# Kernel tuning notes

Measured on AMD Instinct MI355X. Metric: run time of the kernel, lower is better.

The kernel has to match this reference:

```python
import jax, jax.numpy as jnp
import numpy as np

N = 32768       # nodes
IN = 256        # in_channels
D = 128         # out_channels (per-head dim)
H = 4           # num_heads
M = 4           # num_reps (seeds per partition)
KP = 128        # number of partitions
S = N // KP     # partition size (equal-size partitions)
SCALE = float(np.sqrt(D))


def _linear_init(key, fan_in, fan_out):
    # torch nn.Linear default: U(-1/sqrt(fan_in), 1/sqrt(fan_in)) for W and b
    kw, kb = jax.random.split(key)
    bound = 1.0 / np.sqrt(fan_in)
    w = jax.random.uniform(kw, (fan_in, fan_out), jnp.float32, -bound, bound)
    b = jax.random.uniform(kb, (fan_out,), jnp.float32, -bound, bound)
    return w, b


def setup_inputs() -> dict:
    key = jax.random.key(0)
    k0, k1, k2, k3, k4 = jax.random.split(key, 5)
    x = jax.random.normal(k0, (N, IN), jnp.float32)
    # equal-size disjoint partitions: [KP, S] index array covering 0..N-1
    partition_indices = jnp.arange(N, dtype=jnp.int32).reshape(KP, S)
    Wq_w, Wq_b = _linear_init(k1, IN, H * D)
    Wk_w, Wk_b = _linear_init(k2, IN, H * D)
    Wv_w, Wv_b = _linear_init(k3, IN, H * D)
    pool_seeds = jax.random.normal(k4, (M, H, D), jnp.float32) * 0.02
    alpha_logit = jnp.float32(0.0)
    beta = jnp.float32(1.0)
    return {
        "x": x, "partition_indices": partition_indices,
        "Wq_w": Wq_w, "Wq_b": Wq_b, "Wk_w": Wk_w, "Wk_b": Wk_b,
        "Wv_w": Wv_w, "Wv_b": Wv_b, "pool_seeds": pool_seeds,
        "alpha_logit": alpha_logit, "beta": beta,
    }


def reference(x, partition_indices, Wq_w, Wq_b, Wk_w, Wk_b, Wv_w, Wv_b,
              pool_seeds, alpha_logit, beta):
    n = x.shape[0]
    Q = (x @ Wq_w + Wq_b).reshape(n, H, D)
    K = (x @ Wk_w + Wk_b).reshape(n, H, D)
    V = (x @ Wv_w + Wv_b).reshape(n, H, D)

    # gather per partition -> [KP, S, H, D]
    Qp = Q[partition_indices]
    Kp = K[partition_indices]
    Vp = V[partition_indices]

    # Fine: exact softmax attention within each partition
    attn_local = jnp.einsum('kphd,kqhd->khpq', Qp, Kp) / SCALE
    attn_local = jax.nn.softmax(attn_local, axis=-1)
    outp = jnp.einsum('khpq,kqhd->kphd', attn_local, Vp)  # [KP,S,H,D]
    # partitions are disjoint -> scatter-set back to node order
    out_local = jnp.zeros((n, H, D), x.dtype).at[partition_indices.reshape(-1)].set(
        outp.reshape(n, H, D))
    x_local = out_local.mean(axis=1)  # [N, D]

    # Coarse: learned seeds pool each partition
    pool_attn = jnp.einsum('mhd,kqhd->kmhq', pool_seeds, Kp) / SCALE
    pool_attn = jax.nn.softmax(pool_attn, axis=-1)
    reps_k = jnp.einsum('kmhq,kqhd->kmhd', pool_attn, Kp).reshape(KP * M, H, D)
    reps_v = jnp.einsum('kmhq,kqhd->kmhd', pool_attn, Vp).reshape(KP * M, H, D)

    # Global cross-attention: every node attends to all partition reps
    cross_attn = jnp.einsum('nhd,rhd->nhr', Q, reps_k) / SCALE
    cross_attn = jax.nn.softmax(cross_attn, axis=-1)
    out_global = jnp.einsum('nhr,rhd->nhd', cross_attn, reps_v)
    x_global = out_global.mean(axis=1)  # [N, D]

    x_self = V.mean(axis=1)
    alpha = jax.nn.sigmoid(alpha_logit)
    return alpha * x_local + (1.0 - alpha) * x_global + beta * x_self
```

## Files before the change

kernel.cpp:

```cpp
#include <hip/hip_runtime.h>
#include <hip/hip_bf16.h>


#define INV_SCALE 0.08838834764831845f
#define C2EXP 0.12751744f
#define DEFER_THR 90.50966799f

typedef __attribute__((ext_vector_type(8))) short bf16x8;
typedef __attribute__((ext_vector_type(4))) float floatx4;
typedef unsigned short ushort_t;
typedef unsigned int uint32;

#define OFF_Q    0ull
#define OFF_K    33554432ull
#define OFF_V    67108864ull
#define OFF_LOC  100663296ull
#define OFF_RPK  109051904ull
#define OFF_XC   110100480ull
#define OFF_WC   126877696ull
#define OFF_SCAL 127671296ull
#define OFF_FLAG 127671304ull
#define OFF_RVT  127672320ull
#define OFF_GLB  128196608ull

#define WC_WQ 0
#define WC_WK 131072
#define WC_WV 262144
#define WC_BQ 393216
#define WC_BK 393728
#define WC_BV 394240
#define WC_SEED 394752
#define WC_TOT 396800

static __device__ __forceinline__ float bflo(uint32 u) {
  return __uint_as_float(u << 16);
}
static __device__ __forceinline__ float bfhi(uint32 u) {
  return __uint_as_float(u & 0xffff0000u);
}
static __device__ __forceinline__ float bf2f(ushort_t u) {
  return __uint_as_float(((uint32)u) << 16);
}
static __device__ __forceinline__ ushort_t f2bf(float f) {
  uint32 x = __float_as_uint(f);
  uint32 r = x + 0x7fffu + ((x >> 16) & 1u);
  return (ushort_t)(r >> 16);
}
static __device__ __forceinline__ uint32 pack2bf(float a, float b) {
  return (uint32)f2bf(a) | ((uint32)f2bf(b) << 16);
}
static __device__ __forceinline__ uint32 cvtpk(float a, float b) {
  uint32 r;
  asm("v_cvt_pk_bf16_f32 %0, %1, %2" : "=v"(r) : "v"(a), "v"(b));
  return r;
}

static __device__ __forceinline__ void gl2lds16(const ushort_t* g, ushort_t* l) {
  __builtin_amdgcn_global_load_lds(
      (const __attribute__((address_space(1))) void*)g,
      (__attribute__((address_space(3))) void*)l, 16, 0, 0);
}

__global__ __launch_bounds__(64) void k_detect(const uint32* __restrict__ xw,
                                               const ushort_t* __restrict__ betaRaw,
                                               uint32* __restrict__ flags) {
  const int lane = threadIdx.x;
  const uint32 w = xw[lane * 137 + 3];
  const int e = (w >> 7) & 0xff;
  const unsigned long long b = __ballot(e >= 100 && e <= 140);
  if (lane == 0) {
    flags[0] = (__popcll(b) >= 48) ? 1u : 0u;
    flags[1] = (betaRaw[0] != 0) ? 1u : 0u;
  }
}

static __device__ __forceinline__ void conv8(const void* src, long j, int isB,
                                             ushort_t* dst) {
  if (isB) {
    *reinterpret_cast<uint4*>(dst) =
        *reinterpret_cast<const uint4*>(reinterpret_cast<const ushort_t*>(src) + j);
  } else {
    const float* f = reinterpret_cast<const float*>(src) + j;
    const float4 a = *reinterpret_cast<const float4*>(f);
    const float4 b = *reinterpret_cast<const float4*>(f + 4);
    uint4 o;
    o.x = pack2bf(a.x, a.y); o.y = pack2bf(a.z, a.w);
    o.z = pack2bf(b.x, b.y); o.w = pack2bf(b.z, b.w);
    *reinterpret_cast<uint4*>(dst) = o;
  }
}

__global__ __launch_bounds__(256) void k_convert(
    const void* __restrict__ x,
    const void* __restrict__ Wq, const void* __restrict__ bq,
    const void* __restrict__ Wk, const void* __restrict__ bk,
    const void* __restrict__ Wv, const void* __restrict__ bv,
    const void* __restrict__ seeds, const void* __restrict__ alpha,
    const void* __restrict__ beta,
    ushort_t* __restrict__ xc, ushort_t* __restrict__ wc,
    float* __restrict__ scal, const uint32* __restrict__ flags)
{
  const int isB = (int)flags[0];
  const long i8 = ((long)blockIdx.x * 256 + threadIdx.x) * 8;
  if (blockIdx.y == 0) {
    conv8(x, i8, isB, xc + i8);
  } else {
    if (i8 < WC_BQ) {
      const int sel = (int)(i8 >> 17);
      const long local = i8 & 131071;
      const int kk = (int)(local >> 9);
      const int nn = (int)(local & 511);
      const void* src = sel == 0 ? Wq : (sel == 1 ? Wk : Wv);
      ushort_t* dstW = wc + sel * 131072;
#pragma unroll
      for (int j = 0; j < 8; ++j) {
        ushort_t v;
        if (isB) v = reinterpret_cast<const ushort_t*>(src)[local + j];
        else     v = f2bf(reinterpret_cast<const float*>(src)[local + j]);
        dstW[(size_t)(nn + j) * 256 + kk] = v;
      }
    } else if (i8 < WC_TOT) {
      const void* src; long j;
      if (i8 < WC_BK)        { src = bq;    j = i8 - WC_BQ; }
      else if (i8 < WC_BV)   { src = bk;    j = i8 - WC_BK; }
      else if (i8 < WC_SEED) { src = bv;    j = i8 - WC_BV; }
      else                   { src = seeds; j = i8 - WC_SEED; }
      conv8(src, j, isB, wc + i8);
    }
    if (blockIdx.x == 0 && threadIdx.x == 0) {
      const int isBS = (int)flags[1];
      scal[0] = isBS ? bf2f(reinterpret_cast<const ushort_t*>(alpha)[0])
                     : reinterpret_cast<const float*>(alpha)[0];
      scal[1] = isBS ? bf2f(reinterpret_cast<const ushort_t*>(beta)[0])
                     : reinterpret_cast<const float*>(beta)[0];
    }
  }
}

__global__ __launch_bounds__(256) void k_qkv(
    const ushort_t* __restrict__ xc, const ushort_t* __restrict__ wc,
    ushort_t* __restrict__ Qb, ushort_t* __restrict__ Kb, ushort_t* __restrict__ Vb)
{
  const int m0 = blockIdx.x * 64;
  const int tid = threadIdx.x, lane = tid & 63, wv = tid >> 6;
  const int l16 = lane & 15, quad = lane >> 4;

  __shared__ __align__(16) ushort_t Xs[64 * 256];
  __shared__ __align__(16) ushort_t Ws[64 * 256];

#pragma unroll
  for (int i = 0; i < 8; ++i) {
    const int id = tid + 256 * i;
    const int row = id >> 5, c = id & 31;
    uint4 v = *reinterpret_cast<const uint4*>(xc + (size_t)(m0 + row) * 256 + c * 8);
    *reinterpret_cast<uint4*>(&Xs[row * 256 + ((c ^ (row & 7)) << 3)]) = v;
  }

  for (int sel = 0; sel < 3; ++sel) {
    const ushort_t* WT   = wc + sel * 131072;
    const ushort_t* bias = wc + WC_BQ + sel * 512;
    ushort_t* out        = sel == 0 ? Qb : (sel == 1 ? Kb : Vb);
    for (int nc = 0; nc < 8; ++nc) {
      const int n0 = nc * 64;
      __syncthreads();
#pragma unroll
      for (int i = 0; i < 8; ++i) {
        const int id = tid + 256 * i;
        const int row = id >> 5, c = id & 31;
        uint4 v = *reinterpret_cast<const uint4*>(WT + (size_t)(n0 + row) * 256 + c * 8);
        *reinterpret_cast<uint4*>(&Ws[row * 256 + ((c ^ (row & 7)) << 3)]) = v;
      }
      __syncthreads();

      floatx4 acc[4] = {};
      const int arow = wv * 16 + l16;
#pragma unroll
      for (int ks = 0; ks < 8; ++ks) {
        const int ac = ks * 4 + quad;
        bf16x8 a = *reinterpret_cast<const bf16x8*>(&Xs[arow * 256 + ((ac ^ (arow & 7)) << 3)]);
#pragma unroll
        for (int nt = 0; nt < 4; ++nt) {
          const int brow = nt * 16 + l16;
          bf16x8 b = *reinterpret_cast<const bf16x8*>(&Ws[brow * 256 + ((ac ^ (brow & 7)) << 3)]);
          acc[nt] = __builtin_amdgcn_mfma_f32_16x16x32_bf16(a, b, acc[nt], 0, 0, 0);
        }
      }

#pragma unroll
      for (int nt = 0; nt < 4; ++nt) {
        const int col = n0 + nt * 16 + l16;
        const float bf = bf2f(bias[col]);
#pragma unroll
        for (int r = 0; r < 4; ++r) {
          const int row = m0 + wv * 16 + quad * 4 + r;
          out[(size_t)row * 512 + col] = f2bf(acc[nt][r] + bf);
        }
      }
    }
  }
}

__global__ __launch_bounds__(256) void k_pool(
    const ushort_t* __restrict__ Kb, const ushort_t* __restrict__ Vb,
    const int* __restrict__ pidx_all, const ushort_t* __restrict__ wc,
    ushort_t* __restrict__ rpk, ushort_t* __restrict__ rvT)
{
  const int k = blockIdx.x, h = blockIdx.y;
  const int tid = threadIdx.x, lane = tid & 63, wv = tid >> 6;
  const int* pidx = pidx_all + k * 256;

  __shared__ __align__(16) ushort_t SB[128 * 256];
  const uint32* SBU = reinterpret_cast<const uint32*>(SB);

#pragma unroll
  for (int i = 0; i < 16; ++i) {
    const int e8 = tid + 256 * i;
    const int q = e8 >> 4, dc = (e8 & 15) * 8;
    uint4 kv = *reinterpret_cast<const uint4*>(Kb + (size_t)pidx[q] * 512 + h * 128 + dc);
    const ushort_t* ku = reinterpret_cast<const ushort_t*>(&kv);
    const int qp = q >> 1, qb = q & 1;
#pragma unroll
    for (int j = 0; j < 8; ++j) {
      const int d = dc + j;
      SB[d * 256 + (((qp ^ (d & 31)) << 1) | qb)] = ku[j];
    }
  }
  __syncthreads();

  float q00, q01, q10, q11;
  {
    const uint32* ssrc = reinterpret_cast<const uint32*>(wc + WC_SEED + (size_t)(wv * 4 + h) * 128);
    float s00 = 0.f, s01 = 0.f, s10 = 0.f, s11 = 0.f;
#pragma unroll 8
    for (int dc = 0; dc < 64; ++dc) {
      const uint32 qv = ssrc[dc];
      const float a0 = bflo(qv), a1 = bfhi(qv);
      const int d0 = dc * 2, d1 = d0 + 1;
      const int c0 = lane ^ (d0 & 31);
      const int c1 = lane ^ (d1 & 31);
      const uint32 u00 = SBU[d0 * 128 + c0];
      const uint32 u01 = SBU[d0 * 128 + c0 + 64];
      const uint32 u10 = SBU[d1 * 128 + c1];
      const uint32 u11 = SBU[d1 * 128 + c1 + 64];
      s00 += a0 * bflo(u00) + a1 * bflo(u10);
      s01 += a0 * bfhi(u00) + a1 * bfhi(u10);
      s10 += a0 * bflo(u01) + a1 * bflo(u11);
      s11 += a0 * bfhi(u01) + a1 * bfhi(u11);
    }
    s00 *= INV_SCALE; s01 *= INV_SCALE; s10 *= INV_SCALE; s11 *= INV_SCALE;
    float mx = fmaxf(fmaxf(s00, s01), fmaxf(s10, s11));
#pragma unroll
    for (int off = 32; off >= 1; off >>= 1) mx = fmaxf(mx, __shfl_xor(mx, off));
    const float e00 = __expf(s00 - mx), e01 = __expf(s01 - mx);
    const float e10 = __expf(s10 - mx), e11 = __expf(s11 - mx);
    float sm = e00 + e01 + e10 + e11;
#pragma unroll
    for (int off = 32; off >= 1; off >>= 1) sm += __shfl_xor(sm, off);
    const float inv = 1.0f / sm;
    q00 = e00 * inv; q01 = e01 * inv; q10 = e10 * inv; q11 = e11 * inv;
  }

  {
    float rk0 = 0.f, rk1 = 0.f;
    const int d0 = 2 * lane, d1 = 2 * lane + 1;
#pragma unroll 4
    for (int qp = 0; qp < 64; ++qp) {
      const float pa = __shfl(q00, qp), pb = __shfl(q01, qp);
      const float pc = __shfl(q10, qp), pd = __shfl(q11, qp);
      const int c0 = qp ^ (d0 & 31);
      const int c1 = qp ^ (d1 & 31);
      const uint32 u0  = SBU[d0 * 128 + c0];
      const uint32 u0b = SBU[d0 * 128 + c0 + 64];
      const uint32 u1  = SBU[d1 * 128 + c1];
      const uint32 u1b = SBU[d1 * 128 + c1 + 64];
      rk0 += pa * bflo(u0) + pb * bfhi(u0) + pc * bflo(u0b) + pd * bfhi(u0b);
      rk1 += pa * bflo(u1) + pb * bfhi(u1) + pc * bflo(u1b) + pd * bfhi(u1b);
    }
    reinterpret_cast<uint32*>(rpk + ((size_t)((k * 4 + wv) * 4 + h)) * 128)[lane] = pack2bf(rk0, rk1);
  }
  __syncthreads();

#pragma unroll
  for (int i = 0; i < 16; ++i) {
    const int e8 = tid + 256 * i;
    const int q = e8 >> 4, dc = (e8 & 15) * 8;
    uint4 vv = *reinterpret_cast<const uint4*>(Vb + (size_t)pidx[q] * 512 + h * 128 + dc);
    *reinterpret_cast<uint4*>(&SB[q * 128 + dc]) = vv;
  }
  __syncthreads();

  {
    float rv0 = 0.f, rv1 = 0.f;
#pragma unroll 4
    for (int qp = 0; qp < 64; ++qp) {
      const float pa = __shfl(q00, qp), pb = __shfl(q01, qp);
      const float pc = __shfl(q10, qp), pd = __shfl(q11, qp);
      const uint32 v00 = SBU[(2 * qp) * 64 + lane];
      const uint32 v01 = SBU[(2 * qp + 1) * 64 + lane];
      const uint32 v10 = SBU[(128 + 2 * qp) * 64 + lane];
      const uint32 v11 = SBU[(129 + 2 * qp) * 64 + lane];
      rv0 += pa * bflo(v00) + pb * bflo(v01) + pc * bflo(v10) + pd * bflo(v11);
      rv1 += pa * bfhi(v00) + pb * bfhi(v01) + pc * bfhi(v10) + pd * bfhi(v11);
    }
    const int rrep = k * 4 + wv;
    rvT[(size_t)(h * 128 + 2 * lane) * 512 + rrep]     = f2bf(rv0);
    rvT[(size_t)(h * 128 + 2 * lane + 1) * 512 + rrep] = f2bf(rv1);
  }
}

__global__ __launch_bounds__(256) void k_fine(
    const ushort_t* __restrict__ Qb, const ushort_t* __restrict__ Kb,
    const ushort_t* __restrict__ Vb, const int* __restrict__ pidx_all,
    ushort_t* __restrict__ locS)
{
  const int k = blockIdx.x, qg = blockIdx.y;
  const int tid = threadIdx.x, lane = tid & 63, wv = tid >> 6;
  const int l16 = lane & 15, quad = lane >> 4;
  const int* pidx = pidx_all + k * 256;

  __shared__ __align__(16) ushort_t BsK[2][64 * 128];
  __shared__ __align__(16) ushort_t SBV[128 * 64];
  __shared__ __align__(16) ushort_t Ps[4][16 * 72];

  const int qidx = pidx[qg * 64 + wv * 16 + l16];

  const int kRL = lane >> 4;
  const int kCH = lane & 15;
  const int kswz = l16 & 7;

  float accS[8][4];
#pragma unroll
  for (int nt = 0; nt < 8; ++nt)
#pragma unroll
    for (int r = 0; r < 4; ++r) accS[nt][r] = 0.f;

#pragma unroll
  for (int j = 0; j < 4; ++j) {
    const int row = wv * 16 + j * 4 + kRL;
    gl2lds16(Kb + (size_t)pidx[row] * 512 + ((kCH ^ (row & 7)) << 3),
             &BsK[0][(wv * 16 + j * 4) * 128]);
  }
  __syncthreads();

  bf16x8 qf[4];
  floatx4 O[8];
  float m_i = -3e38f, l_i = 0.f;

  for (int idx = 0; idx < 16; ++idx) {
    const int h = idx >> 2, c = idx & 3;
    const int cur = idx & 1;

    if (c == 0) {
      const ushort_t* qrow = Qb + (size_t)qidx * 512 + h * 128 + quad * 8;
#pragma unroll
      for (int ks = 0; ks < 4; ++ks)
        qf[ks] = *reinterpret_cast<const bf16x8*>(qrow + ks * 32);
#pragma unroll
      for (int nt = 0; nt < 8; ++nt) O[nt] = (floatx4){0.f, 0.f, 0.f, 0.f};
      m_i = -3e38f;
      l_i = 0.f;
    }

    if (idx < 15) {
      const int hn = (idx + 1) >> 2, cn = (idx + 1) & 3;
      const int nb = cur ^ 1;
#pragma unroll
      for (int j = 0; j < 4; ++j) {
        const int row = wv * 16 + j * 4 + kRL;
        gl2lds16(Kb + (size_t)pidx[cn * 64 + row] * 512 + hn * 128 +
                     ((kCH ^ (row & 7)) << 3),
                 &BsK[nb][(wv * 16 + j * 4) * 128]);
      }
    }

    floatx4 S[4] = {};
#pragma unroll
    for (int ks = 0; ks < 4; ++ks) {
      const int ac = ks * 4 + quad;
#pragma unroll
      for (int nt = 0; nt < 4; ++nt) {
        bf16x8 b = *reinterpret_cast<const bf16x8*>(
            &BsK[cur][(nt * 16 + l16) * 128 + ((ac ^ kswz) << 3)]);
        S[nt] = __builtin_amdgcn_mfma_f32_16x16x32_bf16(b, qf[ks], S[nt], 0, 0, 0);
      }
    }

    float cm;
    {
      const float m0 = fmaxf(fmaxf(S[0][0], S[0][1]), fmaxf(S[0][2], S[0][3]));
      const float m1 = fmaxf(fmaxf(S[1][0], S[1][1]), fmaxf(S[1][2], S[1][3]));
      const float m2 = fmaxf(fmaxf(S[2][0], S[2][1]), fmaxf(S[2][2], S[2][3]));
      const float m3 = fmaxf(fmaxf(S[3][0], S[3][1]), fmaxf(S[3][2], S[3][3]));
      cm = fmaxf(fmaxf(m0, m1), fmaxf(m2, m3));
      cm = fmaxf(cm, __shfl_xor(cm, 16));
      cm = fmaxf(cm, __shfl_xor(cm, 32));
    }
    if (!__all(cm <= m_i + DEFER_THR)) {
      const float mn = fmaxf(m_i, cm);
      const float sc = exp2f((m_i - mn) * C2EXP);
      m_i = mn;
      l_i *= sc;
      float scR[4];
#pragma unroll
      for (int r = 0; r < 4; ++r) scR[r] = __shfl(sc, quad * 4 + r);
#pragma unroll
      for (int nt = 0; nt < 8; ++nt)
#pragma unroll
        for (int r = 0; r < 4; ++r) O[nt][r] *= scR[r];
    }
    {
      const float mC = m_i * C2EXP;
      float ps = 0.f;
#pragma unroll
      for (int nt = 0; nt < 4; ++nt) {
        const float p0 = exp2f(S[nt][0] * C2EXP - mC);
        const float p1 = exp2f(S[nt][1] * C2EXP - mC);
        const float p2 = exp2f(S[nt][2] * C2EXP - mC);
        const float p3 = exp2f(S[nt][3] * C2EXP - mC);
        ps += (p0 + p1) + (p2 + p3);
        uint2 pk2 = make_uint2(pack2bf(p0, p1), pack2bf(p2, p3));
        *reinterpret_cast<uint2*>(&Ps[wv][l16 * 72 + nt * 16 + quad * 4]) = pk2;
      }
      ps += __shfl_xor(ps, 16);
      ps += __shfl_xor(ps, 32);
      l_i += ps;
    }

    __syncthreads();
#pragma unroll
    for (int i = 0; i < 4; ++i) {
      const int e = tid + 256 * i;
      const int key = e & 63, dc8 = (e >> 6) * 8;
      uint4 vv = *reinterpret_cast<const uint4*>(
          Vb + (size_t)pidx[c * 64 + key] * 512 + h * 128 + dc8);
      const ushort_t* u = reinterpret_cast<const ushort_t*>(&vv);
#pragma unroll
      for (int j = 0; j < 8; ++j) {
        const int d = dc8 + j;
        SBV[d * 64 + (((key >> 3) ^ j) << 3) + (key & 7)] = u[j];
      }
    }
    __syncthreads();

#pragma unroll
    for (int ks = 0; ks < 2; ++ks) {
      bf16x8 a = *reinterpret_cast<const bf16x8*>(&Ps[wv][l16 * 72 + ks * 32 + quad * 8]);
#pragma unroll
      for (int nt = 0; nt < 8; ++nt) {
        const int d = nt * 16 + l16;
        const int q8 = ks * 4 + quad;
        bf16x8 b = *reinterpret_cast<const bf16x8*>(
            &SBV[d * 64 + ((q8 ^ (d & 7)) << 3)]);
        O[nt] = __builtin_amdgcn_mfma_f32_16x16x32_bf16(a, b, O[nt], 0, 0, 0);
      }
    }

    if (c == 3) {
      float invR[4];
#pragma unroll
      for (int r = 0; r < 4; ++r) invR[r] = 1.0f / __shfl(l_i, quad * 4 + r);
#pragma unroll
      for (int nt = 0; nt < 8; ++nt)
#pragma unroll
        for (int r = 0; r < 4; ++r) accS[nt][r] += O[nt][r] * invR[r];
    }

    __syncthreads();
  }

#pragma unroll
  for (int r = 0; r < 4; ++r) {
    const int n = pidx[qg * 64 + wv * 16 + quad * 4 + r];
#pragma unroll
    for (int nt = 0; nt < 8; ++nt)
      locS[(size_t)n * 128 + nt * 16 + l16] = f2bf(accS[nt][r] * 0.25f);
  }
}

__global__ __launch_bounds__(256, 2) void k_cross(
    const ushort_t* __restrict__ Qb, const ushort_t* __restrict__ rpk,
    const ushort_t* __restrict__ rvT, ushort_t* __restrict__ glb)
{
  const int h = blockIdx.y;
  const int n0 = blockIdx.x * 128;
  const int tid = threadIdx.x, lane = tid & 63, wv = tid >> 6;
  const int l16 = lane & 15, quad = lane >> 4;

  __shared__ __align__(16) ushort_t BsK[2][64 * 128];
  __shared__ __align__(16) ushort_t BsV[128 * 64];
  __shared__ __align__(16) ushort_t Ps[2][4][16 * 72];

  bf16x8 qf0[4], qf1[4];
  {
    const ushort_t* q0 =
        Qb + (size_t)(n0 + wv * 16 + l16) * 512 + h * 128 + quad * 8;
    const ushort_t* q1 = q0 + (size_t)64 * 512;
#pragma unroll
    for (int ks = 0; ks < 4; ++ks) {
      qf0[ks] = *reinterpret_cast<const bf16x8*>(q0 + ks * 32);
      qf1[ks] = *reinterpret_cast<const bf16x8*>(q1 + ks * 32);
    }
  }

  const int kRL = lane >> 4;
  const int kCH = lane & 15;
  const int vDL = lane >> 3;
  const int vCH = lane & 7;

  floatx4 O0[8] = {}, O1[8] = {};
  float m0_i = -3e38f, l0_i = 0.f;
  float m1_i = -3e38f, l1_i = 0.f;

  {
#pragma unroll
    for (int j = 0; j < 4; ++j) {
      const int row = wv * 16 + j * 4 + kRL;
      gl2lds16(rpk + (size_t)row * 512 + h * 128 + ((kCH ^ (row & 7)) << 3),
               &BsK[0][(wv * 16 + j * 4) * 128]);
      const int d = wv * 32 + j * 8 + vDL;
      gl2lds16(rvT + (size_t)(h * 128 + d) * 512 + ((vCH ^ (d & 7)) << 3),
               &BsV[(wv * 32 + j * 8) * 64]);
    }
  }
  __syncthreads();

  const int kswz = l16 & 7;

  for (int c = 0; c < 8; ++c) {
    const int cur = c & 1;

    if (c < 7) {
      const int nb = cur ^ 1;
      const int cn = c + 1;
#pragma unroll
      for (int j = 0; j < 4; ++j) {
        const int row = wv * 16 + j * 4 + kRL;
        gl2lds16(rpk + (size_t)(cn * 64 + row) * 512 + h * 128 +
                     ((kCH ^ (row & 7)) << 3),
                 &BsK[nb][(wv * 16 + j * 4) * 128]);
      }
    }

    floatx4 S0[4] = {}, S1[4] = {};
#pragma unroll
    for (int ks = 0; ks < 4; ++ks) {
      const int ac = ks * 4 + quad;
#pragma unroll
      for (int nt = 0; nt < 4; ++nt) {
        bf16x8 b = *reinterpret_cast<const bf16x8*>(
            &BsK[cur][(nt * 16 + l16) * 128 + ((ac ^ kswz) << 3)]);
        S0[nt] = __builtin_amdgcn_mfma_f32_16x16x32_bf16(b, qf0[ks], S0[nt], 0, 0, 0);
        S1[nt] = __builtin_amdgcn_mfma_f32_16x16x32_bf16(b, qf1[ks], S1[nt], 0, 0, 0);
      }
    }

#pragma unroll
    for (int s = 0; s < 2; ++s) {
      floatx4* S      = (s == 0) ? S0 : S1;
      floatx4* O      = (s == 0) ? O0 : O1;
      float& m_i      = (s == 0) ? m0_i : m1_i;
      float& l_i      = (s == 0) ? l0_i : l1_i;

      float cm;
      {
        const float a0 = fmaxf(fmaxf(S[0][0], S[0][1]), fmaxf(S[0][2], S[0][3]));
        const float a1 = fmaxf(fmaxf(S[1][0], S[1][1]), fmaxf(S[1][2], S[1][3]));
        const float a2 = fmaxf(fmaxf(S[2][0], S[2][1]), fmaxf(S[2][2], S[2][3]));
        const float a3 = fmaxf(fmaxf(S[3][0], S[3][1]), fmaxf(S[3][2], S[3][3]));
        cm = fmaxf(fmaxf(a0, a1), fmaxf(a2, a3));
        cm = fmaxf(cm, __shfl_xor(cm, 16));
        cm = fmaxf(cm, __shfl_xor(cm, 32));
      }
      if (!__all(cm <= m_i + DEFER_THR)) {
        const float mn = fmaxf(m_i, cm);
        const float sc = exp2f((m_i - mn) * C2EXP);
        m_i = mn;
        l_i *= sc;
        float scR[4];
#pragma unroll
        for (int r = 0; r < 4; ++r) scR[r] = __shfl(sc, quad * 4 + r);
#pragma unroll
        for (int nt = 0; nt < 8; ++nt)
#pragma unroll
          for (int r = 0; r < 4; ++r) O[nt][r] *= scR[r];
      }
      {
        const float mC = m_i * C2EXP;
        float ps = 0.f;
#pragma unroll
        for (int nt = 0; nt < 4; ++nt) {
          const float p0 = exp2f(S[nt][0] * C2EXP - mC);
          const float p1 = exp2f(S[nt][1] * C2EXP - mC);
          const float p2 = exp2f(S[nt][2] * C2EXP - mC);
          const float p3 = exp2f(S[nt][3] * C2EXP - mC);
          ps += (p0 + p1) + (p2 + p3);
          uint2 pk2 = make_uint2(cvtpk(p0, p1), cvtpk(p2, p3));
          *reinterpret_cast<uint2*>(&Ps[s][wv][l16 * 72 + nt * 16 + quad * 4]) = pk2;
        }
        ps += __shfl_xor(ps, 16);
        ps += __shfl_xor(ps, 32);
        l_i += ps;
      }
    }

    __syncthreads();

#pragma unroll
    for (int ks = 0; ks < 2; ++ks) {
      bf16x8 a0 = *reinterpret_cast<const bf16x8*>(&Ps[0][wv][l16 * 72 + ks * 32 + quad * 8]);
      bf16x8 a1 = *reinterpret_cast<const bf16x8*>(&Ps[1][wv][l16 * 72 + ks * 32 + quad * 8]);
#pragma unroll
      for (int nt = 0; nt < 8; ++nt) {
        const int q8 = ks * 4 + quad;
        bf16x8 b = *reinterpret_cast<const bf16x8*>(
            &BsV[(nt * 16 + l16) * 64 + ((q8 ^ kswz) << 3)]);
        O0[nt] = __builtin_amdgcn_mfma_f32_16x16x32_bf16(a0, b, O0[nt], 0, 0, 0);
        O1[nt] = __builtin_amdgcn_mfma_f32_16x16x32_bf16(a1, b, O1[nt], 0, 0, 0);
      }
    }

    __syncthreads();

    if (c < 7) {
      const int cn = c + 1;
#pragma unroll
      for (int j = 0; j < 4; ++j) {
        const int d = wv * 32 + j * 8 + vDL;
        gl2lds16(rvT + (size_t)(h * 128 + d) * 512 + cn * 64 +
                     ((vCH ^ (d & 7)) << 3),
                 &BsV[(wv * 32 + j * 8) * 64]);
      }
    }
  }

#pragma unroll
  for (int s = 0; s < 2; ++s) {
    const floatx4* O = (s == 0) ? O0 : O1;
    const float l_i  = (s == 0) ? l0_i : l1_i;
    float invR[4];
#pragma unroll
    for (int r = 0; r < 4; ++r) invR[r] = 1.0f / __shfl(l_i, quad * 4 + r);
#pragma unroll
    for (int r = 0; r < 4; ++r) {
      const int n = n0 + s * 64 + wv * 16 + quad * 4 + r;
#pragma unroll
      for (int nt = 0; nt < 8; ++nt)
        glb[(size_t)n * 512 + h * 128 + nt * 16 + l16] = f2bf(O[nt][r] * invR[r]);
    }
  }
}

__global__ __launch_bounds__(256) void k_combine(
    const ushort_t* __restrict__ locS, const ushort_t* __restrict__ glb,
    const ushort_t* __restrict__ Vb, const float* __restrict__ scal,
    float* __restrict__ out)
{
  const int t = blockIdx.x * 256 + threadIdx.x;
  const int n = t >> 6, dp = t & 63;
  const float alpha = 1.0f / (1.0f + __expf(-scal[0]));
  const float beta = scal[1];
  const uint32 lv = reinterpret_cast<const uint32*>(locS)[(size_t)n * 64 + dp];
  float g0 = 0.f, g1 = 0.f, v0 = 0.f, v1 = 0.f;
#pragma unroll
  for (int hh = 0; hh < 4; ++hh) {
    const uint32 gv = *reinterpret_cast<const uint32*>(glb + (size_t)n * 512 + hh * 128 + 2 * dp);
    const uint32 vv = *reinterpret_cast<const uint32*>(Vb + (size_t)n * 512 + hh * 128 + 2 * dp);
    g0 += bflo(gv); g1 += bfhi(gv);
    v0 += bflo(vv); v1 += bfhi(vv);
  }
  const float r0 = alpha * bflo(lv) + (1.0f - alpha) * g0 * 0.25f + beta * v0 * 0.25f;
  const float r1 = alpha * bfhi(lv) + (1.0f - alpha) * g1 * 0.25f + beta * v1 * 0.25f;
  reinterpret_cast<float2*>(out)[(size_t)n * 64 + dp] = make_float2(r0, r1);
}

extern "C" void kernel_launch(void* const* d_in, const int* in_sizes, int n_in,
                              void* d_out, int out_size, void* d_ws, size_t ws_size,
                              hipStream_t stream) {
  const void* x     = d_in[0];
  const int*  pidx  = (const int*)d_in[1];
  const void* Wq    = d_in[2];
  const void* bq    = d_in[3];
  const void* Wk    = d_in[4];
  const void* bk    = d_in[5];
  const void* Wv    = d_in[6];
  const void* bv    = d_in[7];
  const void* seeds = d_in[8];
  const void* al    = d_in[9];
  const void* be    = d_in[10];

  char* ws = (char*)d_ws;
  ushort_t* Qb   = (ushort_t*)(ws + OFF_Q);
  ushort_t* Kb   = (ushort_t*)(ws + OFF_K);
  ushort_t* Vb   = (ushort_t*)(ws + OFF_V);
  ushort_t* locS = (ushort_t*)(ws + OFF_LOC);
  ushort_t* rpk  = (ushort_t*)(ws + OFF_RPK);
  ushort_t* xc   = (ushort_t*)(ws + OFF_XC);
  ushort_t* wc   = (ushort_t*)(ws + OFF_WC);
  float*    scal = (float*)   (ws + OFF_SCAL);
  uint32*   flags= (uint32*)  (ws + OFF_FLAG);
  ushort_t* rvT  = (ushort_t*)(ws + OFF_RVT);
  ushort_t* glb  = (ushort_t*)(ws + OFF_GLB);

  k_detect<<<1, 64, 0, stream>>>((const uint32*)x, (const ushort_t*)be, flags);
  k_convert<<<dim3(4096, 2), 256, 0, stream>>>(x, Wq, bq, Wk, bk, Wv, bv, seeds, al, be,
                                               xc, wc, scal, flags);
  k_qkv<<<512, 256, 0, stream>>>(xc, wc, Qb, Kb, Vb);
  k_pool<<<dim3(128, 4), 256, 0, stream>>>(Kb, Vb, pidx, wc, rpk, rvT);
  k_fine<<<dim3(128, 4), 256, 0, stream>>>(Qb, Kb, Vb, pidx, locS);
  k_cross<<<dim3(256, 4), 256, 0, stream>>>(Qb, rpk, rvT, glb);
  k_combine<<<8192, 256, 0, stream>>>(locS, glb, Vb, scal, (float*)d_out);
}
```

Measured before the change: 315.5 us.

## Double-buffer weight tiles with async global-to-LDS loads in QKV GEMM

```diff
diff --git a/kernel.cpp b/kernel.cpp
--- a/kernel.cpp
+++ b/kernel.cpp
@@ -144,59 +144,71 @@
   const int m0 = blockIdx.x * 64;
   const int tid = threadIdx.x, lane = tid & 63, wv = tid >> 6;
   const int l16 = lane & 15, quad = lane >> 4;
-
-  __shared__ __align__(16) ushort_t Xs[64 * 256];
-  __shared__ __align__(16) ushort_t Ws[64 * 256];
-
-#pragma unroll
-  for (int i = 0; i < 8; ++i) {
-    const int id = tid + 256 * i;
-    const int row = id >> 5, c = id & 31;
-    uint4 v = *reinterpret_cast<const uint4*>(xc + (size_t)(m0 + row) * 256 + c * 8);
-    *reinterpret_cast<uint4*>(&Xs[row * 256 + ((c ^ (row & 7)) << 3)]) = v;
-  }
-
-  for (int sel = 0; sel < 3; ++sel) {
-    const ushort_t* WT   = wc + sel * 131072;
+  const int kswz = l16 & 7;
+
+  __shared__ __align__(16) ushort_t Ws[2][64 * 256];
+
+  bf16x8 af[8];
+  {
+    const ushort_t* xrow = xc + (size_t)(m0 + wv * 16 + l16) * 256 + quad * 8;
+#pragma unroll
+    for (int ks = 0; ks < 8; ++ks)
+      af[ks] = *reinterpret_cast<const bf16x8*>(xrow + ks * 32);
+  }
+
+  const int wRL = lane >> 5;
+  const int wCH = lane & 31;
+
+#pragma unroll
+  for (int j = 0; j < 8; ++j) {
+    const int row = wv * 16 + j * 2 + wRL;
+    gl2lds16(wc + (size_t)row * 256 + ((wCH ^ (row & 7)) << 3),
+             &Ws[0][(wv * 16 + j * 2) * 256]);
+  }
+  __syncthreads();
+
+  for (int t = 0; t < 24; ++t) {
+    const int cur = t & 1;
+
+    if (t < 23) {
+      const int nb = cur ^ 1;
+      const int tn = t + 1;
+#pragma unroll
+      for (int j = 0; j < 8; ++j) {
+        const int row = wv * 16 + j * 2 + wRL;
+        gl2lds16(wc + (size_t)(tn * 64 + row) * 256 + ((wCH ^ (row & 7)) << 3),
+                 &Ws[nb][(wv * 16 + j * 2) * 256]);
+      }
+    }
+
+    floatx4 acc[4] = {};
+#pragma unroll
+    for (int ks = 0; ks < 8; ++ks) {
+      const int ac = ks * 4 + quad;
+#pragma unroll
+      for (int nt = 0; nt < 4; ++nt) {
+        bf16x8 b = *reinterpret_cast<const bf16x8*>(
+            &Ws[cur][(nt * 16 + l16) * 256 + ((ac ^ kswz) << 3)]);
+        acc[nt] = __builtin_amdgcn_mfma_f32_16x16x32_bf16(af[ks], b, acc[nt], 0, 0, 0);
+      }
+    }
+
+    const int sel = t >> 3, nc = t & 7;
     const ushort_t* bias = wc + WC_BQ + sel * 512;
-    ushort_t* out        = sel == 0 ? Qb : (sel == 1 ? Kb : Vb);
-    for (int nc = 0; nc < 8; ++nc) {
-      const int n0 = nc * 64;
-      __syncthreads();
-#pragma unroll
-      for (int i = 0; i < 8; ++i) {
-        const int id = tid + 256 * i;
-        const int row = id >> 5, c = id & 31;
-        uint4 v = *reinterpret_cast<const uint4*>(WT + (size_t)(n0 + row) * 256 + c * 8);
-        *reinterpret_cast<uint4*>(&Ws[row * 256 + ((c ^ (row & 7)) << 3)]) = v;
-      }
-      __syncthreads();
-
-      floatx4 acc[4] = {};
-      const int arow = wv * 16 + l16;
-#pragma unroll
-      for (int ks = 0; ks < 8; ++ks) {
-        const int ac = ks * 4 + quad;
-        bf16x8 a = *reinterpret_cast<const bf16x8*>(&Xs[arow * 256 + ((ac ^ (arow & 7)) << 3)]);
-#pragma unroll
-        for (int nt = 0; nt < 4; ++nt) {
-          const int brow = nt * 16 + l16;
-          bf16x8 b = *reinterpret_cast<const bf16x8*>(&Ws[brow * 256 + ((ac ^ (brow & 7)) << 3)]);
-          acc[nt] = __builtin_amdgcn_mfma_f32_16x16x32_bf16(a, b, acc[nt], 0, 0, 0);
-        }
-      }
-
-#pragma unroll
-      for (int nt = 0; nt < 4; ++nt) {
-        const int col = n0 + nt * 16 + l16;
-        const float bf = bf2f(bias[col]);
-#pragma unroll
-        for (int r = 0; r < 4; ++r) {
-          const int row = m0 + wv * 16 + quad * 4 + r;
-          out[(size_t)row * 512 + col] = f2bf(acc[nt][r] + bf);
-        }
-      }
-    }
+    ushort_t* out = sel == 0 ? Qb : (sel == 1 ? Kb : Vb);
+    const int n0 = nc * 64;
+#pragma unroll
+    for (int nt = 0; nt < 4; ++nt) {
+      const int col = n0 + nt * 16 + l16;
+      const float bf = bf2f(bias[col]);
+#pragma unroll
+      for (int r = 0; r < 4; ++r) {
+        const int row = m0 + wv * 16 + quad * 4 + r;
+        out[(size_t)row * 512 + col] = f2bf(acc[nt][r] + bf);
+      }
+    }
+
+    __syncthreads();
   }
 }
 
```

Measured after the change: 305.7 us (median of 2 runs). -3.1%, faster.
